# Kernel tuning notes

Hardware: AMD Instinct MI355X
Metric: run time of the kernel (lower is better)

The kernel has to match this reference:

```python
import jax, jax.numpy as jnp
import numpy as np
import math

B, S, D = 4, 4096, 1024
H, HD, LK = 16, 64, 256


def setup_inputs() -> dict:
    key = jax.random.key(0)
    ks = jax.random.split(key, 8)
    s = 1.0 / math.sqrt(D)
    return {
        "X": jax.random.normal(ks[0], (B, S, D), jnp.float32),
        "mask": jnp.ones((B, S), jnp.float32),
        "Wq": jax.random.normal(ks[1], (D, H * HD), jnp.float32) * s,
        "bq": jnp.zeros((H * HD,), jnp.float32),
        "Wk": jax.random.normal(ks[2], (D, H * HD), jnp.float32) * s,
        "bk": jnp.zeros((H * HD,), jnp.float32),
        "Wv": jax.random.normal(ks[3], (D, H * HD), jnp.float32) * s,
        "bv": jnp.zeros((H * HD,), jnp.float32),
        "E": jax.random.normal(ks[4], (H, LK, S), jnp.float32) / math.sqrt(LK),
        "Wo": jax.random.normal(ks[5], (H * HD, D), jnp.float32) * s,
        "bo": jnp.zeros((D,), jnp.float32),
    }


def reference(X, mask, Wq, bq, Wk, bk, Wv, bv, E, Wo, bo):
    Bd, Sd, Dd = X.shape

    def split_heads(t):  # [B,S,H*HD] -> [B,H,S,HD]
        return t.reshape(Bd, Sd, H, HD).transpose(0, 2, 1, 3)

    Q = split_heads(X @ Wq + bq)
    K = split_heads(X @ Wk + bk)
    V = split_heads(X @ Wv + bv)

    m = mask[:, None, :, None]  # [B,1,S,1]
    # Low-rank projection along sequence: [H,LK,S] x [B,H,S,HD] -> [B,H,LK,HD]
    Kp = jnp.einsum('hks,bhsd->bhkd', E, K * m)
    Vp = jnp.einsum('hks,bhsd->bhkd', E, V * m)

    dot = jnp.einsum('bhsd,bhkd->bhsk', Q, Kp) / math.sqrt(HD)
    attn = jax.nn.softmax(dot, axis=-1)
    Xo = jnp.einsum('bhsk,bhkd->bhsd', attn, Vp)

    Xo = Xo.transpose(0, 2, 1, 3).reshape(Bd, Sd, H * HD)
    return Xo @ Wo + bo
```

## Files before the change

kernel.cpp:

```cpp
#include <hip/hip_runtime.h>
#include <hip/hip_bf16.h>
#include <stdint.h>

typedef __bf16 bf16_t;
typedef __attribute__((ext_vector_type(8))) __bf16 bf16x8;
typedef __attribute__((ext_vector_type(4))) __bf16 bf16x4;
typedef __attribute__((ext_vector_type(4))) float f32x4;

#define TO_GLB(p) ((const __attribute__((address_space(1))) void*)(p))
#define TO_LDS(p) ((__attribute__((address_space(3))) void*)(p))

__global__ __launch_bounds__(256) void cast2_bf16_kernel(const float* __restrict__ a,
                                                         bf16_t* __restrict__ da,
                                                         const float* __restrict__ b,
                                                         bf16_t* __restrict__ db, int n4) {
  int i = blockIdx.x * 256 + threadIdx.x;
  const float* s = (i < n4) ? a : b;
  bf16_t* d = (i < n4) ? da : db;
  int j = (i < n4) ? i : i - n4;
  float4 v = ((const float4*)s)[j];
  bf16x4 o;
  o[0] = (bf16_t)v.x; o[1] = (bf16_t)v.y; o[2] = (bf16_t)v.z; o[3] = (bf16_t)v.w;
  ((bf16x4*)d)[j] = o;
}

__global__ __launch_bounds__(256) void transpose_cast4(
    const float* __restrict__ W0, const float* __restrict__ W1, const float* __restrict__ W2,
    const float* __restrict__ W3, bf16_t* __restrict__ o0, bf16_t* __restrict__ o1,
    bf16_t* __restrict__ o2, bf16_t* __restrict__ o3) {
  const int RC = 1024;
  __shared__ bf16_t tile[64][72];
  int z = blockIdx.z;
  const float* W = (z == 0) ? W0 : (z == 1) ? W1 : (z == 2) ? W2 : W3;
  bf16_t* out = (z == 0) ? o0 : (z == 1) ? o1 : (z == 2) ? o2 : o3;
  int r0 = blockIdx.y * 64, c0 = blockIdx.x * 64;
  int tid = threadIdx.x;
#pragma unroll
  for (int p = 0; p < 4; ++p) {
    int r = p * 16 + (tid >> 4);
    int c = (tid & 15) * 4;
    float4 v = *(const float4*)(W + (size_t)(r0 + r) * RC + c0 + c);
    tile[r][c + 0] = (bf16_t)v.x; tile[r][c + 1] = (bf16_t)v.y;
    tile[r][c + 2] = (bf16_t)v.z; tile[r][c + 3] = (bf16_t)v.w;
  }
  __syncthreads();
#pragma unroll
  for (int p = 0; p < 4; ++p) {
    int c = p * 16 + (tid >> 4);
    int r = (tid & 15) * 4;
    bf16x4 o;
    o[0] = tile[r + 0][c]; o[1] = tile[r + 1][c];
    o[2] = tile[r + 2][c]; o[3] = tile[r + 3][c];
    *(bf16x4*)(out + (size_t)(c0 + c) * RC + r0 + r) = o;
  }
}


#define STAGE_A(s, h, k0v)                                                                  \
  do {                                                                                      \
    _Pragma("unroll") for (int it_ = 0; it_ < 2; ++it_) {                                   \
      int brow_ = it_ * 128 + (h) * 64 + (wv << 3);                                         \
      int row_ = brow_ + (lane >> 3);                                                       \
      int cc_ = (lane & 7) ^ (lane >> 3);                                                   \
      const bf16_t* ga_ = Ab + (size_t)row_ * K + (k0v) + cc_ * 8;                          \
      __builtin_amdgcn_global_load_lds(TO_GLB(ga_), TO_LDS(Asl##s + brow_ * 64), 16, 0, 0); \
    }                                                                                       \
  } while (0)

#define STAGE_B(s, h, k0v)                                                                  \
  do {                                                                                      \
    _Pragma("unroll") for (int it_ = 0; it_ < 2; ++it_) {                                   \
      int brow_ = (it_ * 2 + (wv >> 2)) * 64 + (h) * 32 + ((wv & 3) << 3);                  \
      int row_ = brow_ + (lane >> 3);                                                       \
      int cc_ = (lane & 7) ^ (lane >> 3);                                                   \
      const bf16_t* gb_ = Bb + (size_t)row_ * K + (k0v) + cc_ * 8;                          \
      __builtin_amdgcn_global_load_lds(TO_GLB(gb_), TO_LDS(Bsl##s + brow_ * 64), 16, 0, 0); \
    }                                                                                       \
  } while (0)

#define VM4 asm volatile("s_waitcnt vmcnt(4)" ::: "memory")
#define VMNONE (void)0

#define PHASE(s, mh, nh, STAGE_STMT, VMC)                                                   \
  do {                                                                                      \
    bf16x8 af_[2][4], bf_[2][2];                                                            \
    _Pragma("unroll") for (int kk_ = 0; kk_ < 2; ++kk_) {                                   \
      _Pragma("unroll") for (int t_ = 0; t_ < 4; ++t_) {                                    \
        int ra_ = wm * 128 + (mh) * 64 + t_ * 16 + m_in;                                    \
        af_[kk_][t_] =                                                                      \
            *(const bf16x8*)(Asl##s + ra_ * 64 + (((kk_ * 4 + q) ^ (ra_ & 7)) * 8));        \
      }                                                                                     \
      _Pragma("unroll") for (int n_ = 0; n_ < 2; ++n_) {                                    \
        int rb_ = wn * 64 + (nh) * 32 + n_ * 16 + m_in;                                     \
        bf_[kk_][n_] =                                                                      \
            *(const bf16x8*)(Bsl##s + rb_ * 64 + (((kk_ * 4 + q) ^ (rb_ & 7)) * 8));        \
      }                                                                                     \
    }                                                                                       \
    STAGE_STMT;                                                                             \
    VMC;                                                                                    \
    __builtin_amdgcn_s_barrier();                                                           \
    asm volatile("s_waitcnt lgkmcnt(0)" ::: "memory");                                      \
    __builtin_amdgcn_s_setprio(1);                                                          \
    _Pragma("unroll") for (int kk_ = 0; kk_ < 2; ++kk_)                                     \
        _Pragma("unroll") for (int t_ = 0; t_ < 4; ++t_)                                    \
            _Pragma("unroll") for (int n_ = 0; n_ < 2; ++n_)                                \
                acc[(mh) * 4 + t_][(nh) * 2 + n_] = __builtin_amdgcn_mfma_f32_16x16x32_bf16( \
                    af_[kk_][t_], bf_[kk_][n_], acc[(mh) * 4 + t_][(nh) * 2 + n_], 0, 0, 0); \
    __builtin_amdgcn_s_setprio(0);                                                          \
    __builtin_amdgcn_s_barrier();                                                           \
  } while (0)

__global__ __launch_bounds__(512) void gemm_bt_8ph(
    const bf16_t* __restrict__ A, const bf16_t* __restrict__ B, int K, int mode,
    const float* __restrict__ bq, const float* __restrict__ bk, const float* __restrict__ bv,
    const float* __restrict__ mask,
    bf16_t* __restrict__ Q, bf16_t* __restrict__ KT, bf16_t* __restrict__ VT,
    const float* __restrict__ bo, float* __restrict__ out) {
  int tid = threadIdx.x;
  int lane = tid & 63, wv = tid >> 6;
  int wm = wv >> 2, wn = wv & 3;
  int q = lane >> 4, m_in = lane & 15;
  int nwg = gridDim.x, cpx = nwg >> 3;
  int bid = blockIdx.x;
  int wgid = (bid & 7) * cpx + (bid >> 3);
  int bm = wgid & 63, bn = wgid >> 6;
  size_t m0 = (size_t)bm * 256;
  size_t n0 = (size_t)bn * 256;
  const bf16_t* Ab = A + m0 * K;
  const bf16_t* Bb = B + n0 * K;
  __shared__ __align__(16) bf16_t Asl0[16384];
  __shared__ __align__(16) bf16_t Asl1[16384];
  __shared__ __align__(16) bf16_t Bsl0[16384];
  __shared__ __align__(16) bf16_t Bsl1[16384];

  f32x4 acc[8][4];
  f32x4 z = {0.f, 0.f, 0.f, 0.f};
#pragma unroll
  for (int mt = 0; mt < 8; ++mt)
#pragma unroll
    for (int nt = 0; nt < 4; ++nt) acc[mt][nt] = z;

  int NT = K >> 6;
  int NI = NT >> 1;

  STAGE_A(0, 0, 0); STAGE_B(0, 0, 0); STAGE_A(0, 1, 0); STAGE_B(0, 1, 0);
  STAGE_A(1, 0, 64); STAGE_B(1, 0, 64);
  asm volatile("s_waitcnt vmcnt(4)" ::: "memory");
  __builtin_amdgcn_s_barrier();

  for (int i = 0; i < NI; ++i) {
    int kt = 2 * i;
    int k1 = (kt + 1) * 64;
    int k2 = (kt + 2 < NT) ? (kt + 2) * 64 : 0;
    int k3 = (kt + 3 < NT) ? (kt + 3) * 64 : 0;
    PHASE(0, 0, 0, STAGE_A(1, 1, k1), VMNONE);
    PHASE(0, 0, 1, STAGE_B(1, 1, k1), VMNONE);
    PHASE(0, 1, 0, STAGE_A(0, 0, k2), VMNONE);
    PHASE(0, 1, 1, STAGE_B(0, 0, k2), VM4);
    PHASE(1, 0, 0, STAGE_A(0, 1, k2), VMNONE);
    PHASE(1, 0, 1, STAGE_B(0, 1, k2), VMNONE);
    PHASE(1, 1, 0, STAGE_A(1, 0, k3), VMNONE);
    PHASE(1, 1, 1, STAGE_B(1, 0, k3), VM4);
  }
  asm volatile("s_waitcnt vmcnt(0)" ::: "memory");

  if (mode == 0) {
#pragma unroll
    for (int mt = 0; mt < 8; ++mt) {
      int mbase = (int)m0 + wm * 128 + mt * 16 + q * 4;
      int b = mbase >> 12, s = mbase & 4095;
      float mk[4];
#pragma unroll
      for (int r = 0; r < 4; ++r) mk[r] = mask[b * 4096 + s + r];
#pragma unroll
      for (int nt = 0; nt < 4; ++nt) {
        int nG = (int)n0 + wn * 64 + nt * 16 + m_in;
        int proj = nG >> 10, c = nG & 1023, h = c >> 6, hd = c & 63;
        const float* bp = (proj == 0) ? bq : ((proj == 1) ? bk : bv);
        float bias = bp[c];
        if (proj == 0) {
#pragma unroll
          for (int r = 0; r < 4; ++r)
            Q[((size_t)(b * 16 + h) * 4096 + s + r) * 64 + hd] = (bf16_t)(acc[mt][nt][r] + bias);
        } else {
          bf16_t* dst = (proj == 1) ? KT : VT;
          bf16x4 v;
#pragma unroll
          for (int r = 0; r < 4; ++r) v[r] = (bf16_t)((acc[mt][nt][r] + bias) * mk[r]);
          *(bf16x4*)(dst + ((size_t)(b * 16 + h) * 64 + hd) * 4096 + s) = v;
        }
      }
    }
  } else {
#pragma unroll
    for (int mt = 0; mt < 8; ++mt) {
      int t = (int)m0 + wm * 128 + mt * 16 + q * 4;
#pragma unroll
      for (int nt = 0; nt < 4; ++nt) {
        int nG = (int)n0 + wn * 64 + nt * 16 + m_in;
        float bias = bo[nG];
#pragma unroll
        for (int r = 0; r < 4; ++r) out[(size_t)(t + r) * 1024 + nG] = acc[mt][nt][r] + bias;
      }
    }
  }
}

__global__ __launch_bounds__(512) void gemm2_kernel(
    const bf16_t* __restrict__ E, const bf16_t* __restrict__ KT, const bf16_t* __restrict__ VT,
    float* __restrict__ Pp) {
  int tid = threadIdx.x, lane = tid & 63, wv = tid >> 6;
  int wm = wv >> 1, wn = wv & 1;
  int q = lane >> 4, m_in = lane & 15;
  int mt0 = blockIdx.x;
  int bh = blockIdx.y;
  int kv = blockIdx.z >> 2, kc = blockIdx.z & 3;
  int h = bh & 15;
  const bf16_t* Ab = E + (size_t)h * 256 * 4096 + (size_t)mt0 * 128 * 4096 + kc * 1024;
  const bf16_t* Bb = (kv ? VT : KT) + (size_t)bh * 64 * 4096 + kc * 1024;
  __shared__ __align__(16) bf16_t As[2 * 128 * 64];
  __shared__ __align__(16) bf16_t Bs[2 * 64 * 64];

  f32x4 acc[2][2];
  f32x4 z = {0.f, 0.f, 0.f, 0.f};
#pragma unroll
  for (int mt = 0; mt < 2; ++mt)
#pragma unroll
    for (int nt = 0; nt < 2; ++nt) acc[mt][nt] = z;

  for (int k0 = 0; k0 < 1024; k0 += 128) {
#pragma unroll
    for (int it = 0; it < 4; ++it) {
      int l = it * 512 + tid;
      int kkb = l >> 10, row = (l >> 3) & 127, cc = (l & 7) ^ (row & 7);
      const bf16_t* ga = Ab + (size_t)row * 4096 + k0 + kkb * 64 + cc * 8;
      __builtin_amdgcn_global_load_lds(TO_GLB(ga), TO_LDS(As + (it * 512 + wv * 64) * 8), 16, 0, 0);
    }
#pragma unroll
    for (int it = 0; it < 2; ++it) {
      int l = it * 512 + tid;
      int kkb = l >> 9, row = (l >> 3) & 63, cc = (l & 7) ^ (row & 7);
      const bf16_t* gb = Bb + (size_t)row * 4096 + k0 + kkb * 64 + cc * 8;
      __builtin_amdgcn_global_load_lds(TO_GLB(gb), TO_LDS(Bs + (it * 512 + wv * 64) * 8), 16, 0, 0);
    }
    __syncthreads();
#pragma unroll
    for (int kk4 = 0; kk4 < 4; ++kk4) {
      int kkb = kk4 >> 1, qq = (kk4 & 1) * 4 + q;
      bf16x8 af[2], bfr[2];
#pragma unroll
      for (int mt = 0; mt < 2; ++mt) {
        int ra = wm * 32 + mt * 16 + m_in;
        af[mt] = *(const bf16x8*)(As + kkb * 8192 + ra * 64 + ((qq ^ (ra & 7)) * 8));
      }
#pragma unroll
      for (int nt = 0; nt < 2; ++nt) {
        int rb = wn * 32 + nt * 16 + m_in;
        bfr[nt] = *(const bf16x8*)(Bs + kkb * 4096 + rb * 64 + ((qq ^ (rb & 7)) * 8));
      }
#pragma unroll
      for (int mt = 0; mt < 2; ++mt)
#pragma unroll
        for (int nt = 0; nt < 2; ++nt)
          acc[mt][nt] = __builtin_amdgcn_mfma_f32_16x16x32_bf16(af[mt], bfr[nt], acc[mt][nt], 0, 0, 0);
    }
    __syncthreads();
  }

  float* P = Pp + ((size_t)(bh * 2 + kv) * 4 + kc) * 16384;
#pragma unroll
  for (int mt = 0; mt < 2; ++mt) {
    int lk = mt0 * 128 + wm * 32 + mt * 16 + q * 4;
#pragma unroll
    for (int nt = 0; nt < 2; ++nt) {
      int hd = wn * 32 + nt * 16 + m_in;
#pragma unroll
      for (int r = 0; r < 4; ++r) P[(size_t)(lk + r) * 64 + hd] = acc[mt][nt][r];
    }
  }
}

__global__ __launch_bounds__(256) void gemm2_reduce(const float* __restrict__ Pp,
                                                    bf16_t* __restrict__ Kp,
                                                    bf16_t* __restrict__ VpT) {
  int bh = blockIdx.x, kv = blockIdx.y;
  int tid = threadIdx.x;
  const float* P = Pp + ((size_t)(bh * 2 + kv) * 4) * 16384;
#pragma unroll
  for (int it = 0; it < 16; ++it) {
    int e4 = it * 256 + tid;
    f32x4 s = *(const f32x4*)(P + e4 * 4);
    f32x4 s1 = *(const f32x4*)(P + 16384 + e4 * 4);
    f32x4 s2 = *(const f32x4*)(P + 32768 + e4 * 4);
    f32x4 s3 = *(const f32x4*)(P + 49152 + e4 * 4);
    s += s1; s += s2; s += s3;
    if (kv == 0) {
      bf16x4 v;
#pragma unroll
      for (int r = 0; r < 4; ++r) v[r] = (bf16_t)s[r];
      *(bf16x4*)(Kp + (size_t)bh * 16384 + e4 * 4) = v;
    } else {
      int lk = (e4 * 4) >> 6, hd = (e4 * 4) & 63;
      bf16_t* d = VpT + (size_t)bh * 16384 + lk;
#pragma unroll
      for (int r = 0; r < 4; ++r) d[(size_t)(hd + r) * 256] = (bf16_t)s[r];
    }
  }
}

__global__ __launch_bounds__(256) void attn_kernel(
    const bf16_t* __restrict__ Q, const bf16_t* __restrict__ Kp, const bf16_t* __restrict__ VpT,
    bf16_t* __restrict__ Xo) {
  int tid = threadIdx.x, lane = tid & 63, wv = tid >> 6;
  int q = lane >> 4, m_in = lane & 15;
  int s0 = blockIdx.x * 64;
  int bh = blockIdx.y;
  int b = bh >> 4, h = bh & 15;
  const bf16_t* Qb = Q + ((size_t)bh * 4096 + s0 + wv * 16) * 64;
  const bf16_t* Kpb = Kp + (size_t)bh * 16384;
  const bf16_t* Vb = VpT + (size_t)bh * 16384;
  __shared__ __align__(16) bf16_t buf[16384];

#pragma unroll
  for (int it = 0; it < 8; ++it) {
    int l = it * 256 + tid;
    int row = l >> 3, cc = (l & 7) ^ (row & 7);
    const bf16_t* g = Kpb + row * 64 + cc * 8;
    __builtin_amdgcn_global_load_lds(TO_GLB(g), TO_LDS(buf + (it * 256 + wv * 64) * 8), 16, 0, 0);
  }
  bf16x8 aq[2];
#pragma unroll
  for (int ks = 0; ks < 2; ++ks) aq[ks] = *(const bf16x8*)(Qb + (size_t)m_in * 64 + ks * 32 + q * 8);
  __syncthreads();

  f32x4 sc[16];
  f32x4 z = {0.f, 0.f, 0.f, 0.f};
#pragma unroll
  for (int nt = 0; nt < 16; ++nt) sc[nt] = z;
#pragma unroll
  for (int nt = 0; nt < 16; ++nt)
#pragma unroll
    for (int ks = 0; ks < 2; ++ks) {
      int nb = nt * 16 + m_in, qq = ks * 4 + q;
      bf16x8 kb = *(const bf16x8*)(buf + nb * 64 + ((qq ^ (nb & 7)) * 8));
      sc[nt] = __builtin_amdgcn_mfma_f32_16x16x32_bf16(aq[ks], kb, sc[nt], 0, 0, 0);
    }

  float mx[4], sm[4];
#pragma unroll
  for (int r = 0; r < 4; ++r) mx[r] = -1e30f;
#pragma unroll
  for (int nt = 0; nt < 16; ++nt)
#pragma unroll
    for (int r = 0; r < 4; ++r) {
      float t = sc[nt][r] * 0.125f;
      sc[nt][r] = t;
      mx[r] = fmaxf(mx[r], t);
    }
#pragma unroll
  for (int off = 1; off < 16; off <<= 1)
#pragma unroll
    for (int r = 0; r < 4; ++r) mx[r] = fmaxf(mx[r], __shfl_xor(mx[r], off));
#pragma unroll
  for (int r = 0; r < 4; ++r) sm[r] = 0.f;
#pragma unroll
  for (int nt = 0; nt < 16; ++nt)
#pragma unroll
    for (int r = 0; r < 4; ++r) {
      float e = __expf(sc[nt][r] - mx[r]);
      sc[nt][r] = e;
      sm[r] += e;
    }
#pragma unroll
  for (int off = 1; off < 16; off <<= 1)
#pragma unroll
    for (int r = 0; r < 4; ++r) sm[r] += __shfl_xor(sm[r], off);
  float inv[4];
#pragma unroll
  for (int r = 0; r < 4; ++r) inv[r] = 1.0f / sm[r];

  __syncthreads();

  bf16_t* Pw = buf + wv * 4096;
#pragma unroll
  for (int nt = 0; nt < 16; ++nt) {
    int cw = nt * 2 + (m_in >> 3);
#pragma unroll
    for (int r = 0; r < 4; ++r) {
      int rp = q * 4 + r;
      int sw = (((cw ^ (rp & 7)) << 3) | (m_in & 7));
      Pw[rp * 256 + sw] = (bf16_t)(sc[nt][r] * inv[r]);
    }
  }
  bf16x8 pa[8];
#pragma unroll
  for (int ks = 0; ks < 8; ++ks) {
    int c = ks * 4 + q;
    pa[ks] = *(const bf16x8*)(Pw + m_in * 256 + ((c ^ (m_in & 7)) << 3));
  }
  __syncthreads();

#pragma unroll
  for (int it = 0; it < 8; ++it) {
    int l = it * 256 + tid;
    int row = l >> 5, cc = l & 31;
    int src_cc = (cc & 24) | ((cc ^ row) & 7);
    const bf16_t* g = Vb + row * 256 + src_cc * 8;
    __builtin_amdgcn_global_load_lds(TO_GLB(g), TO_LDS(buf + (it * 256 + wv * 64) * 8), 16, 0, 0);
  }
  __syncthreads();

  f32x4 o[4];
#pragma unroll
  for (int nt = 0; nt < 4; ++nt) o[nt] = z;
#pragma unroll
  for (int nt = 0; nt < 4; ++nt)
#pragma unroll
    for (int ks = 0; ks < 8; ++ks) {
      int nb = nt * 16 + m_in, qq = ks * 4 + q;
      int p = (qq & 24) | ((qq ^ nb) & 7);
      bf16x8 vb = *(const bf16x8*)(buf + nb * 256 + p * 8);
      o[nt] = __builtin_amdgcn_mfma_f32_16x16x32_bf16(pa[ks], vb, o[nt], 0, 0, 0);
    }

#pragma unroll
  for (int nt = 0; nt < 4; ++nt)
#pragma unroll
    for (int r = 0; r < 4; ++r)
      Xo[((size_t)b * 4096 + s0 + wv * 16 + q * 4 + r) * 1024 + h * 64 + nt * 16 + m_in] =
          (bf16_t)o[nt][r];
}

extern "C" void kernel_launch(void* const* d_in, const int* in_sizes, int n_in,
                              void* d_out, int out_size, void* d_ws, size_t ws_size,
                              hipStream_t stream) {
  const float* X = (const float*)d_in[0];
  const float* mask = (const float*)d_in[1];
  const float* Wq = (const float*)d_in[2];
  const float* bq = (const float*)d_in[3];
  const float* Wk = (const float*)d_in[4];
  const float* bk = (const float*)d_in[5];
  const float* Wv = (const float*)d_in[6];
  const float* bv = (const float*)d_in[7];
  const float* E = (const float*)d_in[8];
  const float* Wo = (const float*)d_in[9];
  const float* bo = (const float*)d_in[10];
  float* out = (float*)d_out;

  char* ws = (char*)d_ws;
  const size_t SZ = 33554432;
  bf16_t* Xb = (bf16_t*)(ws);
  float* Pp = (float*)(ws);
  bf16_t* Eb = (bf16_t*)(ws + SZ);
  bf16_t* Qb = (bf16_t*)(ws + 2 * SZ);
  bf16_t* KT = (bf16_t*)(ws + 3 * SZ);
  bf16_t* VT = (bf16_t*)(ws + 4 * SZ);
  bf16_t* Kp = (bf16_t*)(ws + 5 * SZ);
  bf16_t* VpT = (bf16_t*)(ws + 5 * SZ + 8388608);
  bf16_t* WqkvT = (bf16_t*)(ws + 5 * SZ + 2 * 8388608);
  bf16_t* WoT = (bf16_t*)(ws + 5 * SZ + 2 * 8388608 + 6291456);
  bf16_t* Xo = Xb;

  cast2_bf16_kernel<<<32768, 256, 0, stream>>>(X, Xb, E, Eb, 4194304);
  transpose_cast4<<<dim3(16, 16, 4), 256, 0, stream>>>(
      Wq, Wk, Wv, Wo, WqkvT, WqkvT + 1048576, WqkvT + 2097152, WoT);

  gemm_bt_8ph<<<768, 512, 0, stream>>>(Xb, WqkvT, 1024, 0, bq, bk, bv, mask,
                                       Qb, KT, VT, nullptr, nullptr);
  gemm2_kernel<<<dim3(2, 64, 8), 512, 0, stream>>>(Eb, KT, VT, Pp);
  gemm2_reduce<<<dim3(64, 2), 256, 0, stream>>>(Pp, Kp, VpT);
  attn_kernel<<<dim3(64, 64), 256, 0, stream>>>(Qb, Kp, VpT, Xo);
  gemm_bt_8ph<<<256, 512, 0, stream>>>(Xo, WoT, 1024, 1, nullptr, nullptr, nullptr,
                                       nullptr, nullptr, nullptr, nullptr, bo, out);
}
```

Before: 491.0 us.

## Reuse LDS fragments across GEMM phases and drop workgroup swizzle

Restructures the 8-phase GEMM loop so each k-tile loads the A fragment once per half and keeps both B fragment halves in registers, instead of reloading A and B fragments from LDS in every phase. This cuts LDS read traffic per k-tile. The last phase skips its LDS wait because no new fragments are loaded. It also sets launch_bounds min-blocks to 2 and removes the XCD-aware block index remapping, which may reduce L2 locality across chiplets and raises register pressure.

```diff
diff --git a/kernel.cpp b/kernel.cpp
--- a/kernel.cpp
+++ b/kernel.cpp
@@ -79,38 +79,50 @@
   } while (0)
 
 #define VM4 asm volatile("s_waitcnt vmcnt(4)" ::: "memory")
-#define VMNONE (void)0
-
-#define PHASE(s, mh, nh, STAGE_STMT, VMC)                                                   \
-  do {                                                                                      \
-    bf16x8 af_[2][4], bf_[2][2];                                                            \
-    _Pragma("unroll") for (int kk_ = 0; kk_ < 2; ++kk_) {                                   \
-      _Pragma("unroll") for (int t_ = 0; t_ < 4; ++t_) {                                    \
-        int ra_ = wm * 128 + (mh) * 64 + t_ * 16 + m_in;                                    \
-        af_[kk_][t_] =                                                                      \
-            *(const bf16x8*)(Asl##s + ra_ * 64 + (((kk_ * 4 + q) ^ (ra_ & 7)) * 8));        \
-      }                                                                                     \
-      _Pragma("unroll") for (int n_ = 0; n_ < 2; ++n_) {                                    \
-        int rb_ = wn * 64 + (nh) * 32 + n_ * 16 + m_in;                                     \
-        bf_[kk_][n_] =                                                                      \
-            *(const bf16x8*)(Bsl##s + rb_ * 64 + (((kk_ * 4 + q) ^ (rb_ & 7)) * 8));        \
-      }                                                                                     \
+#define BARRIER __builtin_amdgcn_s_barrier()
+#define LGKM0 asm volatile("s_waitcnt lgkmcnt(0)" ::: "memory")
+
+#define LOAD_AF(s, mh)                                                                      \
+  do {                                                                                      \
+    _Pragma("unroll") for (int kk_ = 0; kk_ < 2; ++kk_)                                     \
+        _Pragma("unroll") for (int t_ = 0; t_ < 4; ++t_) {                                  \
+      int ra_ = wm * 128 + (mh) * 64 + t_ * 16 + m_in;                                      \
+      af[kk_][t_] = *(const bf16x8*)(Asl##s + ra_ * 64 + (((kk_ * 4 + q) ^ (ra_ & 7)) * 8)); \
     }                                                                                       \
-    STAGE_STMT;                                                                             \
-    VMC;                                                                                    \
-    __builtin_amdgcn_s_barrier();                                                           \
-    asm volatile("s_waitcnt lgkmcnt(0)" ::: "memory");                                      \
+  } while (0)
+
+#define LOAD_BF(s, nh, dst)                                                                 \
+  do {                                                                                      \
+    _Pragma("unroll") for (int kk_ = 0; kk_ < 2; ++kk_)                                     \
+        _Pragma("unroll") for (int n_ = 0; n_ < 2; ++n_) {                                  \
+      int rb_ = wn * 64 + (nh) * 32 + n_ * 16 + m_in;                                       \
+      dst[kk_][n_] = *(const bf16x8*)(Bsl##s + rb_ * 64 + (((kk_ * 4 + q) ^ (rb_ & 7)) * 8)); \
+    }                                                                                       \
+  } while (0)
+
+#define MFMA_Q(mh, nh, bfr)                                                                 \
+  do {                                                                                      \
     __builtin_amdgcn_s_setprio(1);                                                          \
     _Pragma("unroll") for (int kk_ = 0; kk_ < 2; ++kk_)                                     \
         _Pragma("unroll") for (int t_ = 0; t_ < 4; ++t_)                                    \
             _Pragma("unroll") for (int n_ = 0; n_ < 2; ++n_)                                \
                 acc[(mh) * 4 + t_][(nh) * 2 + n_] = __builtin_amdgcn_mfma_f32_16x16x32_bf16( \
-                    af_[kk_][t_], bf_[kk_][n_], acc[(mh) * 4 + t_][(nh) * 2 + n_], 0, 0, 0); \
+                    af[kk_][t_], bfr[kk_][n_], acc[(mh) * 4 + t_][(nh) * 2 + n_], 0, 0, 0);  \
     __builtin_amdgcn_s_setprio(0);                                                          \
-    __builtin_amdgcn_s_barrier();                                                           \
-  } while (0)
-
-__global__ __launch_bounds__(512) void gemm_bt_8ph(
+  } while (0)
+
+#define KTILE(s, ST1, ST2, ST3, ST4)                                                        \
+  do {                                                                                      \
+    LOAD_AF(s, 0); LOAD_BF(s, 0, bf0);                                                      \
+    ST1; BARRIER; LGKM0; MFMA_Q(0, 0, bf0); BARRIER;                                        \
+    LOAD_BF(s, 1, bf1);                                                                     \
+    ST2; BARRIER; LGKM0; MFMA_Q(0, 1, bf1); BARRIER;                                        \
+    LOAD_AF(s, 1);                                                                          \
+    ST3; BARRIER; LGKM0; MFMA_Q(1, 0, bf0); BARRIER;                                        \
+    ST4; VM4; BARRIER; MFMA_Q(1, 1, bf1); BARRIER;                                          \
+  } while (0)
+
+__global__ __launch_bounds__(512, 2) void gemm_bt_8ph(
     const bf16_t* __restrict__ A, const bf16_t* __restrict__ B, int K, int mode,
     const float* __restrict__ bq, const float* __restrict__ bk, const float* __restrict__ bv,
     const float* __restrict__ mask,
@@ -120,10 +132,8 @@
   int lane = tid & 63, wv = tid >> 6;
   int wm = wv >> 2, wn = wv & 3;
   int q = lane >> 4, m_in = lane & 15;
-  int nwg = gridDim.x, cpx = nwg >> 3;
   int bid = blockIdx.x;
-  int wgid = (bid & 7) * cpx + (bid >> 3);
-  int bm = wgid & 63, bn = wgid >> 6;
+  int bm = bid & 63, bn = bid >> 6;
   size_t m0 = (size_t)bm * 256;
   size_t n0 = (size_t)bn * 256;
   const bf16_t* Ab = A + m0 * K;
@@ -134,6 +144,7 @@
   __shared__ __align__(16) bf16_t Bsl1[16384];
 
   f32x4 acc[8][4];
+  bf16x8 af[2][4], bf0[2][2], bf1[2][2];
   f32x4 z = {0.f, 0.f, 0.f, 0.f};
 #pragma unroll
   for (int mt = 0; mt < 8; ++mt)
@@ -153,14 +164,8 @@
     int k1 = (kt + 1) * 64;
     int k2 = (kt + 2 < NT) ? (kt + 2) * 64 : 0;
     int k3 = (kt + 3 < NT) ? (kt + 3) * 64 : 0;
-    PHASE(0, 0, 0, STAGE_A(1, 1, k1), VMNONE);
-    PHASE(0, 0, 1, STAGE_B(1, 1, k1), VMNONE);
-    PHASE(0, 1, 0, STAGE_A(0, 0, k2), VMNONE);
-    PHASE(0, 1, 1, STAGE_B(0, 0, k2), VM4);
-    PHASE(1, 0, 0, STAGE_A(0, 1, k2), VMNONE);
-    PHASE(1, 0, 1, STAGE_B(0, 1, k2), VMNONE);
-    PHASE(1, 1, 0, STAGE_A(1, 0, k3), VMNONE);
-    PHASE(1, 1, 1, STAGE_B(1, 0, k3), VM4);
+    KTILE(0, STAGE_A(1, 1, k1), STAGE_B(1, 1, k1), STAGE_A(0, 0, k2), STAGE_B(0, 0, k2));
+    KTILE(1, STAGE_A(0, 1, k2), STAGE_B(0, 1, k2), STAGE_A(1, 0, k3), STAGE_B(1, 0, k3));
   }
   asm volatile("s_waitcnt vmcnt(0)" ::: "memory");
 
```

New measurement: 473.1 us. 3.7% less time.
